# Optimization experiments

Measured on AMD Instinct MI355X. Metric: run time of the kernel, lower is better.

## Reference

```python
import jax, jax.numpy as jnp
import numpy as np

B, N, C, D, K, H = 32, 4096, 128, 64, 8, 128  # batch, tokens, in_dim, slot_dim, num_slots, mlp hidden
SCALE = D ** -0.5
EPS = 1e-8
ITERS = 3


def _ln(x, g, b):
    m = jnp.mean(x, axis=-1, keepdims=True)
    v = jnp.var(x, axis=-1, keepdims=True)
    return (x - m) * jax.lax.rsqrt(v + 1e-5) * g + b


def _gru(x, h, wih, whh, bih, bhh):
    # torch.nn.GRUCell semantics; x:[M,D], h:[M,D], wih/whh:[3D,D]
    gi = x @ wih.T + bih
    gh = h @ whh.T + bhh
    i_r, i_z, i_n = jnp.split(gi, 3, axis=-1)
    h_r, h_z, h_n = jnp.split(gh, 3, axis=-1)
    r = jax.nn.sigmoid(i_r + h_r)
    z = jax.nn.sigmoid(i_z + h_z)
    n = jnp.tanh(i_n + r * h_n)
    return (1.0 - z) * n + z * h


def setup_inputs() -> dict:
    key = jax.random.key(0)
    ks = jax.random.split(key, 24)
    f32 = jnp.float32

    def rn(i, shape, scale):
        return (jax.random.normal(ks[i], shape, f32) * scale)

    return {
        "feat": jax.random.normal(ks[0], (B, N, C), f32),
        "slot": jax.random.normal(ks[1], (B, K, D), f32),
        "norm_feat_g": jnp.ones((C,), f32), "norm_feat_b": jnp.zeros((C,), f32),
        "Wk": rn(2, (C, D), C ** -0.5), "Wv": rn(3, (C, D), C ** -0.5),
        "q_ln_g": jnp.ones((D,), f32), "q_ln_b": jnp.zeros((D,), f32),
        "Wq": rn(4, (D, D), D ** -0.5),
        "qbg_ln_g": jnp.ones((D,), f32), "qbg_ln_b": jnp.zeros((D,), f32),
        "Wq_bg": rn(5, (D, D), D ** -0.5),
        "gru_wih": rn(6, (3 * D, D), D ** -0.5), "gru_whh": rn(7, (3 * D, D), D ** -0.5),
        "gru_bih": jnp.zeros((3 * D,), f32), "gru_bhh": jnp.zeros((3 * D,), f32),
        "grubg_wih": rn(8, (3 * D, D), D ** -0.5), "grubg_whh": rn(9, (3 * D, D), D ** -0.5),
        "grubg_bih": jnp.zeros((3 * D,), f32), "grubg_bhh": jnp.zeros((3 * D,), f32),
        "res_ln_g": jnp.ones((D,), f32), "res_ln_b": jnp.zeros((D,), f32),
        "res_w1": rn(10, (D, H), D ** -0.5), "res_b1": jnp.zeros((H,), f32),
        "res_w2": rn(11, (H, D), H ** -0.5), "res_b2": jnp.zeros((D,), f32),
        "resbg_ln_g": jnp.ones((D,), f32), "resbg_ln_b": jnp.zeros((D,), f32),
        "resbg_w1": rn(12, (D, H), D ** -0.5), "resbg_b1": jnp.zeros((H,), f32),
        "resbg_w2": rn(13, (H, D), H ** -0.5), "resbg_b2": jnp.zeros((D,), f32),
    }


def reference(feat, slot, norm_feat_g, norm_feat_b, Wk, Wv,
              q_ln_g, q_ln_b, Wq, qbg_ln_g, qbg_ln_b, Wq_bg,
              gru_wih, gru_whh, gru_bih, gru_bhh,
              grubg_wih, grubg_whh, grubg_bih, grubg_bhh,
              res_ln_g, res_ln_b, res_w1, res_b1, res_w2, res_b2,
              resbg_ln_g, resbg_ln_b, resbg_w1, resbg_b1, resbg_w2, resbg_b2):
    # split externally-provided slots (slot is not None branch)
    slot_bg = slot[:, :1, :]   # [B,1,D]   (bg_slot_dim == fg_slot_dim == D)
    slot_fg = slot[:, 1:, :]   # [B,K-1,D]

    x = _ln(feat, norm_feat_g, norm_feat_b)   # [B,N,C]
    k = x @ Wk                                 # [B,N,D]
    v = x @ Wv                                 # [B,N,D]

    attn = None
    for _ in range(ITERS):
        q_fg = _ln(slot_fg, q_ln_g, q_ln_b) @ Wq          # [B,K-1,D]
        q_bg = _ln(slot_bg, qbg_ln_g, qbg_ln_b) @ Wq_bg   # [B,1,D]
        dots_fg = jnp.einsum('bid,bjd->bij', q_fg, k) * SCALE
        dots_bg = jnp.einsum('bid,bjd->bij', q_bg, k) * SCALE
        dots = jnp.concatenate([dots_bg, dots_fg], axis=1)  # [B,K,N]
        attn = jax.nn.softmax(dots, axis=1) + EPS            # softmax over slots
        attn_bg, attn_fg = attn[:, :1, :], attn[:, 1:, :]
        w_bg = attn_bg / jnp.sum(attn_bg, axis=-1, keepdims=True)
        w_fg = attn_fg / jnp.sum(attn_fg, axis=-1, keepdims=True)
        upd_fg = jnp.einsum('bjd,bij->bid', v, w_fg)  # [B,K-1,D]
        upd_bg = jnp.einsum('bjd,bij->bid', v, w_bg)  # [B,1,D]

        s_bg = _gru(upd_bg.reshape(-1, D), slot_bg.reshape(-1, D),
                    grubg_wih, grubg_whh, grubg_bih, grubg_bhh).reshape(B, 1, D)
        slot_bg = s_bg + (jax.nn.relu(_ln(s_bg, resbg_ln_g, resbg_ln_b) @ resbg_w1 + resbg_b1) @ resbg_w2 + resbg_b2)

        s_fg = _gru(upd_fg.reshape(-1, D), slot_fg.reshape(-1, D),
                    gru_wih, gru_whh, gru_bih, gru_bhh).reshape(B, K - 1, D)
        slot_fg = s_fg + (jax.nn.relu(_ln(s_fg, res_ln_g, res_ln_b) @ res_w1 + res_b1) @ res_w2 + res_b2)

    slots = jnp.concatenate([slot_bg, slot_fg], axis=1)  # [B,K,D]
    return slots, attn
```

## Files before the change

### kernel.cpp

```cpp
#include <hip/hip_runtime.h>
#include <hip/hip_bf16.h>

constexpr int BB = 32;
constexpr int NN = 4096;
constexpr int CC = 128;
constexpr int DD = 64;
constexpr int KK = 8;
constexpr int HH = 128;
constexpr float SCALE = 0.125f;
constexpr float EPS_A = 1e-8f;
constexpr float LN_EPS = 1e-5f;

constexpr int NT = 16;
constexpr int TILE_N = 256;

typedef __bf16 bfx8 __attribute__((ext_vector_type(8)));
typedef float f32x4 __attribute__((ext_vector_type(4)));

__device__ inline float wave_sum(float x) {
#pragma unroll
    for (int off = 32; off > 0; off >>= 1) x += __shfl_xor(x, off, 64);
    return x;
}

__device__ inline float sigmoidf_(float x) { return 1.f / (1.f + __expf(-x)); }

__device__ inline unsigned short bf16rne(float x) {
    unsigned u = __float_as_uint(x);
    unsigned r = u + 0x7fffu + ((u >> 16) & 1u);
    return (unsigned short)(r >> 16);
}
__device__ inline float bf16tof(unsigned short h) {
    return __uint_as_float(((unsigned)h) << 16);
}

__global__ __launch_bounds__(256) void k0_prepw(
    const float* __restrict__ Wk, const float* __restrict__ Wv,
    unsigned short* __restrict__ fragW)
{
    const int o = blockIdx.x * 256 + threadIdx.x;
    const int j = o & 7, l = (o >> 3) & 63, nf = (o >> 9) & 7, ks = o >> 12;
    const int c = ks * 32 + ((l >> 4) << 3) + j;
    const int n = nf * 16 + (l & 15);
    const float w = (n < DD) ? Wk[c * DD + n] : Wv[c * DD + (n - DD)];
    fragW[o] = bf16rne(w);
}

__global__ __launch_bounds__(256, 2) void k1_mfma(
    const float* __restrict__ feat, const float* __restrict__ nf_g,
    const float* __restrict__ nf_b, const unsigned short* __restrict__ fragW,
    float* __restrict__ kT, float* __restrict__ vout)
{
    __shared__ unsigned short wlds[16384];
    __shared__ char ubuf[32768];

    const int tid = threadIdx.x, w = tid >> 6, lane = tid & 63;

#pragma unroll
    for (int t = 0; t < 8; t++)
        ((uint4*)wlds)[t * 256 + tid] = ((const uint4*)fragW)[t * 256 + tid];

    const size_t row0 = (size_t)blockIdx.x * 64;
    const float g0 = nf_g[lane], g1 = nf_g[lane + 64];
    const float b0 = nf_b[lane], b1 = nf_b[lane + 64];

    unsigned short* xh_hi = (unsigned short*)ubuf;
    unsigned short* xh_lo = (unsigned short*)(ubuf + 16384);

#pragma unroll 4
    for (int r0 = 0; r0 < 16; r0++) {
        const int r = w * 16 + r0;
        const float* fp = feat + (row0 + r) * CC;
        const float x0 = fp[lane], x1 = fp[lane + 64];
        const float m = wave_sum(x0 + x1) * (1.f / 128.f);
        const float d0 = x0 - m, d1 = x1 - m;
        const float var = wave_sum(d0 * d0 + d1 * d1) * (1.f / 128.f);
        const float rs = rsqrtf(var + LN_EPS);
        const float y0 = d0 * rs * g0 + b0;
        const float y1 = d1 * rs * g1 + b1;
        const int sw = (r & 7) << 4;
        const unsigned short h0 = bf16rne(y0), h1 = bf16rne(y1);
        const unsigned short l0 = bf16rne(y0 - bf16tof(h0));
        const unsigned short l1 = bf16rne(y1 - bf16tof(h1));
        const int o0 = (r * 256 + (((2 * lane)) ^ sw)) >> 1;
        const int o1 = (r * 256 + (((2 * lane + 128)) ^ sw)) >> 1;
        xh_hi[o0] = h0; xh_hi[o1] = h1;
        xh_lo[o0] = l0; xh_lo[o1] = l1;
    }
    __syncthreads();

    f32x4 acc[8];
#pragma unroll
    for (int nf = 0; nf < 8; nf++) acc[nf] = (f32x4){0.f, 0.f, 0.f, 0.f};

    const int arow = w * 16 + (lane & 15);
    const int hi16 = lane >> 4;
    const int asw = (arow & 7) << 4;
#pragma unroll
    for (int ks = 0; ks < 4; ks++) {
        const int abyte = arow * 256 + ((ks * 64 + hi16 * 16) ^ asw);
        const bfx8 ah = __builtin_bit_cast(bfx8, *(const uint4*)(ubuf + abyte));
        const bfx8 al = __builtin_bit_cast(bfx8, *(const uint4*)(ubuf + 16384 + abyte));
#pragma unroll
        for (int nf = 0; nf < 8; nf++) {
            const bfx8 bw = __builtin_bit_cast(
                bfx8, *(const uint4*)(wlds + ((ks * 8 + nf) * 64 + lane) * 8));
            acc[nf] = __builtin_amdgcn_mfma_f32_16x16x32_bf16(ah, bw, acc[nf], 0, 0, 0);
            acc[nf] = __builtin_amdgcn_mfma_f32_16x16x32_bf16(al, bw, acc[nf], 0, 0, 0);
        }
    }
    __syncthreads();

    float* kslds = (float*)ubuf;
    const int trow = w * 16 + (lane >> 4) * 4;
#pragma unroll
    for (int nf = 0; nf < 4; nf++) {
        const int d = nf * 16 + (lane & 15);
#pragma unroll
        for (int reg = 0; reg < 4; reg++)
            kslds[d * 65 + trow + reg] = acc[nf][reg];
    }
    {
        const size_t vbase = (row0 + trow) * DD + (lane & 15);
#pragma unroll
        for (int nf = 4; nf < 8; nf++) {
#pragma unroll
            for (int reg = 0; reg < 4; reg++)
                vout[vbase + (size_t)reg * DD + (nf - 4) * 16] = acc[nf][reg];
        }
    }
    __syncthreads();

    const int b = (int)(row0 >> 12);
    const int n0 = (int)(row0 & 4095);
#pragma unroll
    for (int t = 0; t < 16; t++) {
        const int idx = t * 256 + tid;
        const int d = idx >> 6, nn = idx & 63;
        kT[((size_t)b * DD + d) * NN + n0 + nn] = kslds[d * 65 + nn];
    }
}

__global__ __launch_bounds__(256) void k2_attn(
    const float* __restrict__ kT, const float* __restrict__ v,
    const float* __restrict__ q, float* __restrict__ Upart,
    float* __restrict__ Spart, float* __restrict__ attn_out)
{
    __shared__ float qT[DD][KK];
    __shared__ float al[TILE_N][KK];
    __shared__ float Ur[4][KK * DD];
    __shared__ float Sr[4][KK];

    const int tid = threadIdx.x, wave = tid >> 6, lane = tid & 63;
    const int b = blockIdx.x / NT, tile = blockIdx.x % NT;
    const int n0 = tile * TILE_N;

    for (int t = tid; t < KK * DD; t += 256) qT[t % DD][t / DD] = q[b * KK * DD + t];
    __syncthreads();

    const int n = n0 + wave * 64 + lane;
    const float* kp = kT + (size_t)b * DD * NN + n;
    float kv[DD];
#pragma unroll
    for (int d = 0; d < DD; d++) kv[d] = kp[(size_t)d * NN];

    float dots[KK];
#pragma unroll
    for (int i = 0; i < KK; i++) dots[i] = 0.f;
#pragma unroll
    for (int d = 0; d < DD; d++) {
        const float k_ = kv[d];
        const float4 q0 = *(const float4*)&qT[d][0];
        const float4 q1 = *(const float4*)&qT[d][4];
        dots[0] += k_ * q0.x; dots[1] += k_ * q0.y;
        dots[2] += k_ * q0.z; dots[3] += k_ * q0.w;
        dots[4] += k_ * q1.x; dots[5] += k_ * q1.y;
        dots[6] += k_ * q1.z; dots[7] += k_ * q1.w;
    }
    float m = -1e30f;
#pragma unroll
    for (int i = 0; i < KK; i++) { dots[i] *= SCALE; m = fmaxf(m, dots[i]); }
    float s = 0.f, e[KK];
#pragma unroll
    for (int i = 0; i < KK; i++) { e[i] = __expf(dots[i] - m); s += e[i]; }
    const float inv = 1.f / s;
    float a[KK], sv[KK];
#pragma unroll
    for (int i = 0; i < KK; i++) { a[i] = e[i] * inv + EPS_A; sv[i] = a[i]; }

    const int nl = wave * 64 + lane;
    *(float4*)&al[nl][0] = make_float4(a[0], a[1], a[2], a[3]);
    *(float4*)&al[nl][4] = make_float4(a[4], a[5], a[6], a[7]);
    if (attn_out) {
#pragma unroll
        for (int i = 0; i < KK; i++)
            attn_out[((size_t)b * KK + i) * NN + n] = a[i];
    }
#pragma unroll
    for (int off = 32; off > 0; off >>= 1) {
#pragma unroll
        for (int i = 0; i < KK; i++) sv[i] += __shfl_xor(sv[i], off, 64);
    }
    if (lane == 0) {
#pragma unroll
        for (int i = 0; i < KK; i++) Sr[wave][i] = sv[i];
    }
    __syncthreads();

    const float* vp = v + ((size_t)b * NN + n0 + wave * 64) * DD + lane;
    float vv[64];
#pragma unroll
    for (int t = 0; t < 64; t++) vv[t] = vp[t * DD];

    float U[KK];
#pragma unroll
    for (int i = 0; i < KK; i++) U[i] = 0.f;
#pragma unroll
    for (int t = 0; t < 64; t++) {
        const float vx = vv[t];
        const float4 a0 = *(const float4*)&al[wave * 64 + t][0];
        const float4 a1 = *(const float4*)&al[wave * 64 + t][4];
        U[0] += a0.x * vx; U[1] += a0.y * vx; U[2] += a0.z * vx; U[3] += a0.w * vx;
        U[4] += a1.x * vx; U[5] += a1.y * vx; U[6] += a1.z * vx; U[7] += a1.w * vx;
    }
#pragma unroll
    for (int i = 0; i < KK; i++) Ur[wave][i * DD + lane] = U[i];
    __syncthreads();

    for (int t = tid; t < KK * DD; t += 256) {
        Upart[(size_t)blockIdx.x * KK * DD + t] =
            Ur[0][t] + Ur[1][t] + Ur[2][t] + Ur[3][t];
    }
    if (tid < KK)
        Spart[blockIdx.x * KK + tid] =
            Sr[0][tid] + Sr[1][tid] + Sr[2][tid] + Sr[3][tid];
}

__global__ __launch_bounds__(64) void k3_update(
    const float* __restrict__ Upart, const float* __restrict__ Spart,
    const float* __restrict__ h_in, float* __restrict__ slots_cur,
    float* __restrict__ qout,
    const float* __restrict__ gru_wih, const float* __restrict__ gru_whh,
    const float* __restrict__ gru_bih, const float* __restrict__ gru_bhh,
    const float* __restrict__ gbg_wih, const float* __restrict__ gbg_whh,
    const float* __restrict__ gbg_bih, const float* __restrict__ gbg_bhh,
    const float* __restrict__ res_g, const float* __restrict__ res_b,
    const float* __restrict__ res_w1, const float* __restrict__ res_b1,
    const float* __restrict__ res_w2, const float* __restrict__ res_b2,
    const float* __restrict__ rbg_g, const float* __restrict__ rbg_b,
    const float* __restrict__ rbg_w1, const float* __restrict__ rbg_b1,
    const float* __restrict__ rbg_w2, const float* __restrict__ rbg_b2,
    const float* __restrict__ qln_g, const float* __restrict__ qln_b,
    const float* __restrict__ Wq, const float* __restrict__ qbg_g,
    const float* __restrict__ qbg_b, const float* __restrict__ Wqbg,
    float* __restrict__ out_slots, int do_update)
{
    const int blk = blockIdx.x;
    const int b = blk >> 3, i = blk & 7, lane = threadIdx.x;
    __shared__ float upd_s[DD], h_s[DD], lnx_s[DD], h1_s[HH];

    const float h = h_in[(size_t)blk * DD + lane];
    h_s[lane] = h;

    if (do_update) {
        float ssum = (lane < NT) ? Spart[(size_t)(b * NT + lane) * KK + i] : 0.f;
        ssum = wave_sum(ssum);
        float us = 0.f;
#pragma unroll
        for (int p = 0; p < NT; p++)
            us += Upart[((size_t)(b * NT + p) * KK + i) * DD + lane];
        upd_s[lane] = us / ssum;
    }
    __syncthreads();

    float newh = h;
    if (do_update) {
        const float* wih = i ? gru_wih : gbg_wih;
        const float* whh = i ? gru_whh : gbg_whh;
        const float* bih = i ? gru_bih : gbg_bih;
        const float* bhh = i ? gru_bhh : gbg_bhh;
        float gi3[3], gh3[3];
#pragma unroll
        for (int gg = 0; gg < 3; gg++) {
            const int j = gg * DD + lane;
            float si = bih[j], sh = bhh[j];
#pragma unroll
            for (int d4 = 0; d4 < 16; d4++) {
                const float4 wi = *(const float4*)&wih[j * DD + d4 * 4];
                const float4 wh = *(const float4*)&whh[j * DD + d4 * 4];
                const float4 ud = *(const float4*)&upd_s[d4 * 4];
                const float4 hd = *(const float4*)&h_s[d4 * 4];
                si += wi.x * ud.x + wi.y * ud.y + wi.z * ud.z + wi.w * ud.w;
                sh += wh.x * hd.x + wh.y * hd.y + wh.z * hd.z + wh.w * hd.w;
            }
            gi3[gg] = si; gh3[gg] = sh;
        }
        const float r = sigmoidf_(gi3[0] + gh3[0]);
        const float z = sigmoidf_(gi3[1] + gh3[1]);
        const float ng = tanhf(gi3[2] + r * gh3[2]);
        const float tmp = (1.f - z) * ng + z * h;

        const float m = wave_sum(tmp) * (1.f / DD);
        const float dv = tmp - m;
        const float var = wave_sum(dv * dv) * (1.f / DD);
        const float lnx = dv * rsqrtf(var + LN_EPS) * (i ? res_g : rbg_g)[lane] +
                          (i ? res_b : rbg_b)[lane];
        lnx_s[lane] = lnx;
        __syncthreads();
        const float* w1 = i ? res_w1 : rbg_w1;
        const float* b1 = i ? res_b1 : rbg_b1;
#pragma unroll
        for (int t = 0; t < 2; t++) {
            const int j = t * DD + lane;
            float sacc = b1[j];
#pragma unroll 16
            for (int d = 0; d < DD; d++) sacc += lnx_s[d] * w1[d * HH + j];
            h1_s[j] = fmaxf(sacc, 0.f);
        }
        __syncthreads();
        const float* w2 = i ? res_w2 : rbg_w2;
        float o = (i ? res_b2 : rbg_b2)[lane];
#pragma unroll 16
        for (int j = 0; j < HH; j++) o += h1_s[j] * w2[j * DD + lane];
        newh = tmp + o;
    }

    slots_cur[(size_t)blk * DD + lane] = newh;
    if (out_slots) out_slots[(size_t)blk * DD + lane] = newh;

    const float m2 = wave_sum(newh) * (1.f / DD);
    const float d2 = newh - m2;
    const float v2 = wave_sum(d2 * d2) * (1.f / DD);
    const float lq = d2 * rsqrtf(v2 + LN_EPS) * (i ? qln_g : qbg_g)[lane] +
                     (i ? qln_b : qbg_b)[lane];
    __syncthreads();
    lnx_s[lane] = lq;
    __syncthreads();
    const float* W = i ? Wq : Wqbg;
    float qv = 0.f;
#pragma unroll 16
    for (int e = 0; e < DD; e++) qv += lnx_s[e] * W[e * DD + lane];
    qout[(size_t)blk * DD + lane] = qv;
}

extern "C" void kernel_launch(void* const* d_in, const int* in_sizes, int n_in,
                              void* d_out, int out_size, void* d_ws, size_t ws_size,
                              hipStream_t stream)
{
    const float* feat    = (const float*)d_in[0];
    const float* slot_in = (const float*)d_in[1];
    const float* nf_g    = (const float*)d_in[2];
    const float* nf_b    = (const float*)d_in[3];
    const float* Wk      = (const float*)d_in[4];
    const float* Wv      = (const float*)d_in[5];
    const float* qln_g   = (const float*)d_in[6];
    const float* qln_b   = (const float*)d_in[7];
    const float* Wq      = (const float*)d_in[8];
    const float* qbg_g   = (const float*)d_in[9];
    const float* qbg_b   = (const float*)d_in[10];
    const float* Wqbg    = (const float*)d_in[11];
    const float* gru_wih = (const float*)d_in[12];
    const float* gru_whh = (const float*)d_in[13];
    const float* gru_bih = (const float*)d_in[14];
    const float* gru_bhh = (const float*)d_in[15];
    const float* gbg_wih = (const float*)d_in[16];
    const float* gbg_whh = (const float*)d_in[17];
    const float* gbg_bih = (const float*)d_in[18];
    const float* gbg_bhh = (const float*)d_in[19];
    const float* res_g   = (const float*)d_in[20];
    const float* res_b   = (const float*)d_in[21];
    const float* res_w1  = (const float*)d_in[22];
    const float* res_b1  = (const float*)d_in[23];
    const float* res_w2  = (const float*)d_in[24];
    const float* res_b2  = (const float*)d_in[25];
    const float* rbg_g   = (const float*)d_in[26];
    const float* rbg_b   = (const float*)d_in[27];
    const float* rbg_w1  = (const float*)d_in[28];
    const float* rbg_b1  = (const float*)d_in[29];
    const float* rbg_w2  = (const float*)d_in[30];
    const float* rbg_b2  = (const float*)d_in[31];

    float* out = (float*)d_out;
    char* ws = (char*)d_ws;
    size_t off = 0;
    unsigned short* fragW = (unsigned short*)(ws + off); off += 16384 * 2;
    off = (off + 255) & ~(size_t)255;
    float* kT    = (float*)(ws + off); off += (size_t)BB * DD * NN * 4;
    float* v     = (float*)(ws + off); off += (size_t)BB * NN * DD * 4;
    float* q     = (float*)(ws + off); off += (size_t)BB * KK * DD * 4;
    float* slots = (float*)(ws + off); off += (size_t)BB * KK * DD * 4;
    float* Upart = (float*)(ws + off); off += (size_t)BB * NT * KK * DD * 4;
    float* Spart = (float*)(ws + off); off += (size_t)BB * NT * KK * 4;
    if (off > ws_size) return;

    float* out_slots = out;
    float* out_attn  = out + BB * KK * DD;

    k0_prepw<<<64, 256, 0, stream>>>(Wk, Wv, fragW);

    k3_update<<<BB * KK, 64, 0, stream>>>(
        Upart, Spart, slot_in, slots, q,
        gru_wih, gru_whh, gru_bih, gru_bhh, gbg_wih, gbg_whh, gbg_bih, gbg_bhh,
        res_g, res_b, res_w1, res_b1, res_w2, res_b2,
        rbg_g, rbg_b, rbg_w1, rbg_b1, rbg_w2, rbg_b2,
        qln_g, qln_b, Wq, qbg_g, qbg_b, Wqbg, nullptr, 0);

    k1_mfma<<<BB * NN / 64, 256, 0, stream>>>(feat, nf_g, nf_b, fragW, kT, v);

    for (int it = 0; it < 3; it++) {
        k2_attn<<<BB * NT, 256, 0, stream>>>(
            kT, v, q, Upart, Spart, it == 2 ? out_attn : nullptr);
        k3_update<<<BB * KK, 64, 0, stream>>>(
            Upart, Spart, slots, slots, q,
            gru_wih, gru_whh, gru_bih, gru_bhh, gbg_wih, gbg_whh, gbg_bih, gbg_bhh,
            res_g, res_b, res_w1, res_b1, res_w2, res_b2,
            rbg_g, rbg_b, rbg_w1, rbg_b1, rbg_w2, rbg_b2,
            qln_g, qln_b, Wq, qbg_g, qbg_b, Wqbg,
            it == 2 ? out_slots : nullptr, 1);
    }
}
```

Before: 273.2 us.

## Restructure attention, projection and slot-update kernels for wider parallelism

The attention kernel becomes one 64-thread wave per 64-token tile, using readlane broadcasts instead of LDS for q and attention weights, with partials written per wave (64 tiles per batch). The update kernel uses 384 threads so GRU gate matvecs run in parallel over transposed weights precomputed by a new prep kernel, and the MLP is split across threads. The K/V projection kernel drops the LDS weight staging, reads fragments straight from global, uses vectorized row loads and packed stores, and asks for higher occupancy. The trade-off is more partials to reduce and global reads of the weight fragments in the MFMA loop.

```diff
diff --git a/kernel.cpp b/kernel.cpp
--- a/kernel.cpp
+++ b/kernel.cpp
@@ -11,8 +11,7 @@
 constexpr float EPS_A = 1e-8f;
 constexpr float LN_EPS = 1e-5f;
 
-constexpr int NT = 16;
-constexpr int TILE_N = 256;
+constexpr int NTIL = 64;
 
 typedef __bf16 bfx8 __attribute__((ext_vector_type(8)));
 typedef float f32x4 __attribute__((ext_vector_type(4)));
@@ -21,6 +20,10 @@
 #pragma unroll
     for (int off = 32; off > 0; off >>= 1) x += __shfl_xor(x, off, 64);
     return x;
+}
+
+__device__ inline float lane_bcast(float v, int src) {
+    return __uint_as_float(__builtin_amdgcn_readlane(__float_as_uint(v), src));
 }
 
 __device__ inline float sigmoidf_(float x) { return 1.f / (1.f + __expf(-x)); }
@@ -46,46 +49,48 @@
     fragW[o] = bf16rne(w);
 }
 
-__global__ __launch_bounds__(256, 2) void k1_mfma(
+__global__ __launch_bounds__(256) void k0_prepg(
+    const float* __restrict__ fg_ih, const float* __restrict__ fg_hh,
+    const float* __restrict__ bg_ih, const float* __restrict__ bg_hh,
+    float* __restrict__ wT)
+{
+    const int o = blockIdx.x * 256 + threadIdx.x;
+    const int m = o / (DD * 3 * DD);
+    const int rem = o % (DD * 3 * DD);
+    const int d = rem / (3 * DD), j = rem % (3 * DD);
+    const float* W = (m == 0) ? fg_ih : (m == 1) ? fg_hh : (m == 2) ? bg_ih : bg_hh;
+    wT[o] = W[j * DD + d];
+}
+
+__global__ __launch_bounds__(256, 4) void k1_mfma(
     const float* __restrict__ feat, const float* __restrict__ nf_g,
     const float* __restrict__ nf_b, const unsigned short* __restrict__ fragW,
     float* __restrict__ kT, float* __restrict__ vout)
 {
-    __shared__ unsigned short wlds[16384];
     __shared__ char ubuf[32768];
 
     const int tid = threadIdx.x, w = tid >> 6, lane = tid & 63;
-
-#pragma unroll
-    for (int t = 0; t < 8; t++)
-        ((uint4*)wlds)[t * 256 + tid] = ((const uint4*)fragW)[t * 256 + tid];
-
     const size_t row0 = (size_t)blockIdx.x * 64;
-    const float g0 = nf_g[lane], g1 = nf_g[lane + 64];
-    const float b0 = nf_b[lane], b1 = nf_b[lane + 64];
-
-    unsigned short* xh_hi = (unsigned short*)ubuf;
-    unsigned short* xh_lo = (unsigned short*)(ubuf + 16384);
+
+    const float2 g2 = *(const float2*)&nf_g[2 * lane];
+    const float2 b2 = *(const float2*)&nf_b[2 * lane];
 
 #pragma unroll 4
     for (int r0 = 0; r0 < 16; r0++) {
         const int r = w * 16 + r0;
-        const float* fp = feat + (row0 + r) * CC;
-        const float x0 = fp[lane], x1 = fp[lane + 64];
-        const float m = wave_sum(x0 + x1) * (1.f / 128.f);
-        const float d0 = x0 - m, d1 = x1 - m;
+        const float2 x2 = *(const float2*)&feat[(row0 + r) * CC + 2 * lane];
+        const float m = wave_sum(x2.x + x2.y) * (1.f / 128.f);
+        const float d0 = x2.x - m, d1 = x2.y - m;
         const float var = wave_sum(d0 * d0 + d1 * d1) * (1.f / 128.f);
         const float rs = rsqrtf(var + LN_EPS);
-        const float y0 = d0 * rs * g0 + b0;
-        const float y1 = d1 * rs * g1 + b1;
-        const int sw = (r & 7) << 4;
+        const float y0 = d0 * rs * g2.x + b2.x;
+        const float y1 = d1 * rs * g2.y + b2.y;
         const unsigned short h0 = bf16rne(y0), h1 = bf16rne(y1);
         const unsigned short l0 = bf16rne(y0 - bf16tof(h0));
         const unsigned short l1 = bf16rne(y1 - bf16tof(h1));
-        const int o0 = (r * 256 + (((2 * lane)) ^ sw)) >> 1;
-        const int o1 = (r * 256 + (((2 * lane + 128)) ^ sw)) >> 1;
-        xh_hi[o0] = h0; xh_hi[o1] = h1;
-        xh_lo[o0] = l0; xh_lo[o1] = l1;
+        const int off = r * 256 + ((4 * lane) ^ ((r & 7) << 4));
+        *(unsigned*)(ubuf + off) = (unsigned)h0 | ((unsigned)h1 << 16);
+        *(unsigned*)(ubuf + 16384 + off) = (unsigned)l0 | ((unsigned)l1 << 16);
     }
     __syncthreads();
 
@@ -104,7 +109,7 @@
 #pragma unroll
         for (int nf = 0; nf < 8; nf++) {
             const bfx8 bw = __builtin_bit_cast(
-                bfx8, *(const uint4*)(wlds + ((ks * 8 + nf) * 64 + lane) * 8));
+                bfx8, *(const uint4*)(fragW + ((ks * 8 + nf) * 64 + lane) * 8));
             acc[nf] = __builtin_amdgcn_mfma_f32_16x16x32_bf16(ah, bw, acc[nf], 0, 0, 0);
             acc[nf] = __builtin_amdgcn_mfma_f32_16x16x32_bf16(al, bw, acc[nf], 0, 0, 0);
         }
@@ -141,24 +146,20 @@
     }
 }
 
-__global__ __launch_bounds__(256) void k2_attn(
+__global__ __launch_bounds__(64) void k2_attn(
     const float* __restrict__ kT, const float* __restrict__ v,
     const float* __restrict__ q, float* __restrict__ Upart,
     float* __restrict__ Spart, float* __restrict__ attn_out)
 {
-    __shared__ float qT[DD][KK];
-    __shared__ float al[TILE_N][KK];
-    __shared__ float Ur[4][KK * DD];
-    __shared__ float Sr[4][KK];
-
-    const int tid = threadIdx.x, wave = tid >> 6, lane = tid & 63;
-    const int b = blockIdx.x / NT, tile = blockIdx.x % NT;
-    const int n0 = tile * TILE_N;
-
-    for (int t = tid; t < KK * DD; t += 256) qT[t % DD][t / DD] = q[b * KK * DD + t];
-    __syncthreads();
-
-    const int n = n0 + wave * 64 + lane;
+    const int blk = blockIdx.x;
+    const int b = blk >> 6, tile = blk & 63;
+    const int lane = threadIdx.x;
+    const int n = (tile << 6) + lane;
+
+    float qreg[KK];
+#pragma unroll
+    for (int i = 0; i < KK; i++) qreg[i] = q[((size_t)b * KK + i) * DD + lane];
+
     const float* kp = kT + (size_t)b * DD * NN + n;
     float kv[DD];
 #pragma unroll
@@ -170,12 +171,9 @@
 #pragma unroll
     for (int d = 0; d < DD; d++) {
         const float k_ = kv[d];
-        const float4 q0 = *(const float4*)&qT[d][0];
-        const float4 q1 = *(const float4*)&qT[d][4];
-        dots[0] += k_ * q0.x; dots[1] += k_ * q0.y;
-        dots[2] += k_ * q0.z; dots[3] += k_ * q0.w;
-        dots[4] += k_ * q1.x; dots[5] += k_ * q1.y;
-        dots[6] += k_ * q1.z; dots[7] += k_ * q1.w;
+#pragma unroll
+        for (int i = 0; i < KK; i++)
+            dots[i] += k_ * lane_bcast(qreg[i], d);
     }
     float m = -1e30f;
 #pragma unroll
@@ -188,9 +186,6 @@
 #pragma unroll
     for (int i = 0; i < KK; i++) { a[i] = e[i] * inv + EPS_A; sv[i] = a[i]; }
 
-    const int nl = wave * 64 + lane;
-    *(float4*)&al[nl][0] = make_float4(a[0], a[1], a[2], a[3]);
-    *(float4*)&al[nl][4] = make_float4(a[4], a[5], a[6], a[7]);
     if (attn_out) {
 #pragma unroll
         for (int i = 0; i < KK; i++)
@@ -201,13 +196,9 @@
 #pragma unroll
         for (int i = 0; i < KK; i++) sv[i] += __shfl_xor(sv[i], off, 64);
     }
-    if (lane == 0) {
-#pragma unroll
-        for (int i = 0; i < KK; i++) Sr[wave][i] = sv[i];
-    }
-    __syncthreads();
-
-    const float* vp = v + ((size_t)b * NN + n0 + wave * 64) * DD + lane;
+    if (lane < KK) Spart[(size_t)blk * KK + lane] = sv[lane];
+
+    const float* vp = v + ((size_t)b * NN + (tile << 6)) * DD + lane;
     float vv[64];
 #pragma unroll
     for (int t = 0; t < 64; t++) vv[t] = vp[t * DD];
@@ -218,31 +209,20 @@
 #pragma unroll
     for (int t = 0; t < 64; t++) {
         const float vx = vv[t];
-        const float4 a0 = *(const float4*)&al[wave * 64 + t][0];
-        const float4 a1 = *(const float4*)&al[wave * 64 + t][4];
-        U[0] += a0.x * vx; U[1] += a0.y * vx; U[2] += a0.z * vx; U[3] += a0.w * vx;
-        U[4] += a1.x * vx; U[5] += a1.y * vx; U[6] += a1.z * vx; U[7] += a1.w * vx;
-    }
-#pragma unroll
-    for (int i = 0; i < KK; i++) Ur[wave][i * DD + lane] = U[i];
-    __syncthreads();
-
-    for (int t = tid; t < KK * DD; t += 256) {
-        Upart[(size_t)blockIdx.x * KK * DD + t] =
-            Ur[0][t] + Ur[1][t] + Ur[2][t] + Ur[3][t];
-    }
-    if (tid < KK)
-        Spart[blockIdx.x * KK + tid] =
-            Sr[0][tid] + Sr[1][tid] + Sr[2][tid] + Sr[3][tid];
-}
-
-__global__ __launch_bounds__(64) void k3_update(
+#pragma unroll
+        for (int i = 0; i < KK; i++)
+            U[i] += lane_bcast(a[i], t) * vx;
+    }
+#pragma unroll
+    for (int i = 0; i < KK; i++)
+        Upart[((size_t)blk * KK + i) * DD + lane] = U[i];
+}
+
+__global__ __launch_bounds__(384) void k3_update(
     const float* __restrict__ Upart, const float* __restrict__ Spart,
     const float* __restrict__ h_in, float* __restrict__ slots_cur,
-    float* __restrict__ qout,
-    const float* __restrict__ gru_wih, const float* __restrict__ gru_whh,
+    float* __restrict__ qout, const float* __restrict__ wT,
     const float* __restrict__ gru_bih, const float* __restrict__ gru_bhh,
-    const float* __restrict__ gbg_wih, const float* __restrict__ gbg_whh,
     const float* __restrict__ gbg_bih, const float* __restrict__ gbg_bhh,
     const float* __restrict__ res_g, const float* __restrict__ res_b,
     const float* __restrict__ res_w1, const float* __restrict__ res_b1,
@@ -256,91 +236,122 @@
     float* __restrict__ out_slots, int do_update)
 {
     const int blk = blockIdx.x;
-    const int b = blk >> 3, i = blk & 7, lane = threadIdx.x;
-    __shared__ float upd_s[DD], h_s[DD], lnx_s[DD], h1_s[HH];
-
-    const float h = h_in[(size_t)blk * DD + lane];
-    h_s[lane] = h;
-
+    const int b = blk >> 3, i = blk & 7;
+    const int t = threadIdx.x;
+    const int fg = (i != 0);
+
+    __shared__ float h_s[DD], upd_s[DD], red[4][DD],
+        gih_s[3 * DD], ghh_s[3 * DD], lnx_s[DD], h1_s[HH];
+
+    if (t < DD) h_s[t] = h_in[(size_t)blk * DD + t];
+
+    float sp = 0.f;
     if (do_update) {
-        float ssum = (lane < NT) ? Spart[(size_t)(b * NT + lane) * KK + i] : 0.f;
-        ssum = wave_sum(ssum);
-        float us = 0.f;
-#pragma unroll
-        for (int p = 0; p < NT; p++)
-            us += Upart[((size_t)(b * NT + p) * KK + i) * DD + lane];
-        upd_s[lane] = us / ssum;
-    }
-    __syncthreads();
-
-    float newh = h;
+        if (t < 256) {
+            const int d = t & 63, g = t >> 6;
+            float sacc = 0.f;
+#pragma unroll
+            for (int p = 0; p < 16; p++)
+                sacc += Upart[((size_t)(b * NTIL + g * 16 + p) * KK + i) * DD + d];
+            red[g][d] = sacc;
+        }
+        if (t < 64) {
+            sp = Spart[(size_t)(b * NTIL + t) * KK + i];
+            sp = wave_sum(sp);
+        }
+        __syncthreads();
+        if (t < 64)
+            upd_s[t] = (red[0][t] + red[1][t] + red[2][t] + red[3][t]) / sp;
+        __syncthreads();
+
+        {
+            const int isIH = (t < 3 * DD);
+            const int j = isIH ? t : t - 3 * DD;
+            const float* w = wT + (size_t)((fg ? 0 : 2) + (isIH ? 0 : 1)) * (DD * 3 * DD);
+            const float* xs = isIH ? upd_s : h_s;
+            const float* bias = isIH ? (fg ? gru_bih : gbg_bih)
+                                     : (fg ? gru_bhh : gbg_bhh);
+            float acc = bias[j];
+#pragma unroll
+            for (int d4 = 0; d4 < 16; d4++) {
+                const float4 xv = *(const float4*)&xs[d4 * 4];
+                acc += xv.x * w[(d4 * 4 + 0) * 192 + j];
+                acc += xv.y * w[(d4 * 4 + 1) * 192 + j];
+                acc += xv.z * w[(d4 * 4 + 2) * 192 + j];
+                acc += xv.w * w[(d4 * 4 + 3) * 192 + j];
+            }
+            if (isIH) gih_s[j] = acc; else ghh_s[j] = acc;
+        }
+        __syncthreads();
+    }
+
+    float tmpv = 0.f, newh = 0.f;
     if (do_update) {
-        const float* wih = i ? gru_wih : gbg_wih;
-        const float* whh = i ? gru_whh : gbg_whh;
-        const float* bih = i ? gru_bih : gbg_bih;
-        const float* bhh = i ? gru_bhh : gbg_bhh;
-        float gi3[3], gh3[3];
-#pragma unroll
-        for (int gg = 0; gg < 3; gg++) {
-            const int j = gg * DD + lane;
-            float si = bih[j], sh = bhh[j];
+        if (t < 64) {
+            const float r = sigmoidf_(gih_s[t] + ghh_s[t]);
+            const float z = sigmoidf_(gih_s[DD + t] + ghh_s[DD + t]);
+            const float ng = tanhf(gih_s[2 * DD + t] + r * ghh_s[2 * DD + t]);
+            tmpv = (1.f - z) * ng + z * h_s[t];
+            const float m = wave_sum(tmpv) * (1.f / DD);
+            const float dv = tmpv - m;
+            const float var = wave_sum(dv * dv) * (1.f / DD);
+            lnx_s[t] = dv * rsqrtf(var + LN_EPS) * (fg ? res_g : rbg_g)[t] +
+                       (fg ? res_b : rbg_b)[t];
+        }
+        __syncthreads();
+        if (t < HH) {
+            const float* w1 = fg ? res_w1 : rbg_w1;
+            float acc = (fg ? res_b1 : rbg_b1)[t];
 #pragma unroll
             for (int d4 = 0; d4 < 16; d4++) {
-                const float4 wi = *(const float4*)&wih[j * DD + d4 * 4];
-                const float4 wh = *(const float4*)&whh[j * DD + d4 * 4];
-                const float4 ud = *(const float4*)&upd_s[d4 * 4];
-                const float4 hd = *(const float4*)&h_s[d4 * 4];
-                si += wi.x * ud.x + wi.y * ud.y + wi.z * ud.z + wi.w * ud.w;
-                sh += wh.x * hd.x + wh.y * hd.y + wh.z * hd.z + wh.w * hd.w;
+                const float4 xv = *(const float4*)&lnx_s[d4 * 4];
+                acc += xv.x * w1[(d4 * 4 + 0) * HH + t];
+                acc += xv.y * w1[(d4 * 4 + 1) * HH + t];
+                acc += xv.z * w1[(d4 * 4 + 2) * HH + t];
+                acc += xv.w * w1[(d4 * 4 + 3) * HH + t];
             }
-            gi3[gg] = si; gh3[gg] = sh;
-        }
-        const float r = sigmoidf_(gi3[0] + gh3[0]);
-        const float z = sigmoidf_(gi3[1] + gh3[1]);
-        const float ng = tanhf(gi3[2] + r * gh3[2]);
-        const float tmp = (1.f - z) * ng + z * h;
-
-        const float m = wave_sum(tmp) * (1.f / DD);
-        const float dv = tmp - m;
-        const float var = wave_sum(dv * dv) * (1.f / DD);
-        const float lnx = dv * rsqrtf(var + LN_EPS) * (i ? res_g : rbg_g)[lane] +
-                          (i ? res_b : rbg_b)[lane];
-        lnx_s[lane] = lnx;
+            h1_s[t] = fmaxf(acc, 0.f);
+        }
         __syncthreads();
-        const float* w1 = i ? res_w1 : rbg_w1;
-        const float* b1 = i ? res_b1 : rbg_b1;
-#pragma unroll
-        for (int t = 0; t < 2; t++) {
-            const int j = t * DD + lane;
-            float sacc = b1[j];
-#pragma unroll 16
-            for (int d = 0; d < DD; d++) sacc += lnx_s[d] * w1[d * HH + j];
-            h1_s[j] = fmaxf(sacc, 0.f);
-        }
-        __syncthreads();
-        const float* w2 = i ? res_w2 : rbg_w2;
-        float o = (i ? res_b2 : rbg_b2)[lane];
-#pragma unroll 16
-        for (int j = 0; j < HH; j++) o += h1_s[j] * w2[j * DD + lane];
-        newh = tmp + o;
-    }
-
-    slots_cur[(size_t)blk * DD + lane] = newh;
-    if (out_slots) out_slots[(size_t)blk * DD + lane] = newh;
-
-    const float m2 = wave_sum(newh) * (1.f / DD);
-    const float d2 = newh - m2;
-    const float v2 = wave_sum(d2 * d2) * (1.f / DD);
-    const float lq = d2 * rsqrtf(v2 + LN_EPS) * (i ? qln_g : qbg_g)[lane] +
-                     (i ? qln_b : qbg_b)[lane];
-    __syncthreads();
-    lnx_s[lane] = lq;
-    __syncthreads();
-    const float* W = i ? Wq : Wqbg;
-    float qv = 0.f;
-#pragma unroll 16
-    for (int e = 0; e < DD; e++) qv += lnx_s[e] * W[e * DD + lane];
-    qout[(size_t)blk * DD + lane] = qv;
+        if (t < 64) {
+            const float* w2 = fg ? res_w2 : rbg_w2;
+            float o = (fg ? res_b2 : rbg_b2)[t];
+#pragma unroll
+            for (int j4 = 0; j4 < 32; j4++) {
+                const float4 hv = *(const float4*)&h1_s[j4 * 4];
+                o += hv.x * w2[(j4 * 4 + 0) * DD + t];
+                o += hv.y * w2[(j4 * 4 + 1) * DD + t];
+                o += hv.z * w2[(j4 * 4 + 2) * DD + t];
+                o += hv.w * w2[(j4 * 4 + 3) * DD + t];
+            }
+            newh = tmpv + o;
+        }
+    } else {
+        if (t < 64) newh = h_s[t];
+    }
+
+    if (t < 64) {
+        slots_cur[(size_t)blk * DD + t] = newh;
+        if (out_slots) out_slots[(size_t)blk * DD + t] = newh;
+
+        const float m2 = wave_sum(newh) * (1.f / DD);
+        const float d2 = newh - m2;
+        const float v2 = wave_sum(d2 * d2) * (1.f / DD);
+        lnx_s[t] = d2 * rsqrtf(v2 + LN_EPS) * (fg ? qln_g : qbg_g)[t] +
+                   (fg ? qln_b : qbg_b)[t];
+        __builtin_amdgcn_s_waitcnt(0);
+        const float* W = fg ? Wq : Wqbg;
+        float qv = 0.f;
+#pragma unroll
+        for (int e4 = 0; e4 < 16; e4++) {
+            const float4 xv = *(const float4*)&lnx_s[e4 * 4];
+            qv += xv.x * W[(e4 * 4 + 0) * DD + t];
+            qv += xv.y * W[(e4 * 4 + 1) * DD + t];
+            qv += xv.z * W[(e4 * 4 + 2) * DD + t];
+            qv += xv.w * W[(e4 * 4 + 3) * DD + t];
+        }
+        qout[(size_t)blk * DD + t] = qv;
+    }
 }
 
 extern "C" void kernel_launch(void* const* d_in, const int* in_sizes, int n_in,
@@ -385,22 +396,24 @@
     size_t off = 0;
     unsigned short* fragW = (unsigned short*)(ws + off); off += 16384 * 2;
     off = (off + 255) & ~(size_t)255;
+    float* wT    = (float*)(ws + off); off += 4 * DD * 3 * DD * 4;
     float* kT    = (float*)(ws + off); off += (size_t)BB * DD * NN * 4;
     float* v     = (float*)(ws + off); off += (size_t)BB * NN * DD * 4;
     float* q     = (float*)(ws + off); off += (size_t)BB * KK * DD * 4;
     float* slots = (float*)(ws + off); off += (size_t)BB * KK * DD * 4;
-    float* Upart = (float*)(ws + off); off += (size_t)BB * NT * KK * DD * 4;
-    float* Spart = (float*)(ws + off); off += (size_t)BB * NT * KK * 4;
+    float* Upart = (float*)(ws + off); off += (size_t)BB * NTIL * KK * DD * 4;
+    float* Spart = (float*)(ws + off); off += (size_t)BB * NTIL * KK * 4;
     if (off > ws_size) return;
 
     float* out_slots = out;
     float* out_attn  = out + BB * KK * DD;
 
     k0_prepw<<<64, 256, 0, stream>>>(Wk, Wv, fragW);
-
-    k3_update<<<BB * KK, 64, 0, stream>>>(
-        Upart, Spart, slot_in, slots, q,
-        gru_wih, gru_whh, gru_bih, gru_bhh, gbg_wih, gbg_whh, gbg_bih, gbg_bhh,
+    k0_prepg<<<192, 256, 0, stream>>>(gru_wih, gru_whh, gbg_wih, gbg_whh, wT);
+
+    k3_update<<<BB * KK, 384, 0, stream>>>(
+        Upart, Spart, slot_in, slots, q, wT,
+        gru_bih, gru_bhh, gbg_bih, gbg_bhh,
         res_g, res_b, res_w1, res_b1, res_w2, res_b2,
         rbg_g, rbg_b, rbg_w1, rbg_b1, rbg_w2, rbg_b2,
         qln_g, qln_b, Wq, qbg_g, qbg_b, Wqbg, nullptr, 0);
@@ -408,11 +421,11 @@
     k1_mfma<<<BB * NN / 64, 256, 0, stream>>>(feat, nf_g, nf_b, fragW, kT, v);
 
     for (int it = 0; it < 3; it++) {
-        k2_attn<<<BB * NT, 256, 0, stream>>>(
+        k2_attn<<<BB * NTIL, 64, 0, stream>>>(
             kT, v, q, Upart, Spart, it == 2 ? out_attn : nullptr);
-        k3_update<<<BB * KK, 64, 0, stream>>>(
-            Upart, Spart, slots, slots, q,
-            gru_wih, gru_whh, gru_bih, gru_bhh, gbg_wih, gbg_whh, gbg_bih, gbg_bhh,
+        k3_update<<<BB * KK, 384, 0, stream>>>(
+            Upart, Spart, slots, slots, q, wT,
+            gru_bih, gru_bhh, gbg_bih, gbg_bhh,
             res_g, res_b, res_w1, res_b1, res_w2, res_b2,
             rbg_g, rbg_b, rbg_w1, rbg_b1, rbg_w2, rbg_b2,
             qln_g, qln_b, Wq, qbg_g, qbg_b, Wqbg,
```

Measured after the change: 268.2 us. About the same (-1.8%).
